# Optimization experiments

Measured on AMD Instinct MI355X. Metric: run time of the kernel, lower is better.

The kernel has to match this reference:

```python
import jax, jax.numpy as jnp
import numpy as np

SCALES = (32.0, 64.0, 128.0, 256.0)
RATIOS = (0.5, 1.0, 2.0)
STRIDE = 16
KEEP = 2000          # pre-NMS top-k
TOPK = 300           # post-NMS top-k
MIN_SIZE = 16.0
SCORE_THRESH = 0.05
NMS_THRESH = 0.7


def static_anchors():
    a = []
    for s in SCALES:
        for r in RATIOS:
            w = s * r ** 0.5
            h = s / r ** 0.5
            a.append((-w / 2, -h / 2, w / 2, h / 2))
    return jnp.asarray(a, jnp.float32)  # [12,4]


def generate_anchors(h, w):
    base = static_anchors()
    sx = jnp.arange(w, dtype=jnp.float32) * STRIDE + STRIDE / 2
    sy = jnp.arange(h, dtype=jnp.float32) * STRIDE + STRIDE / 2
    yy, xx = jnp.meshgrid(sy, sx, indexing='ij')
    xs, ys = xx.reshape(-1), yy.reshape(-1)
    shifts = jnp.stack((xs, ys, xs, ys), axis=1)            # [HW,4]
    return (base[None, :, :] + shifts[:, None, :]).reshape(-1, 4)  # [HW*12,4]


def apply_deltas(anchors, d):
    # bbox reg weights are all 1.0
    aw = anchors[..., 2] - anchors[..., 0]
    ah = anchors[..., 3] - anchors[..., 1]
    ax = anchors[..., 0] + aw * 0.5
    ay = anchors[..., 1] + ah * 0.5
    x = ax + d[..., 0] * aw
    y = ay + d[..., 1] * ah
    w = aw * jnp.exp(d[..., 2])
    h = ah * jnp.exp(d[..., 3])
    return jnp.stack((x - w * 0.5, y - h * 0.5, x + w * 0.5, y + h * 0.5), axis=-1)


def conv2d(x, w, b, pad):
    y = jax.lax.conv_general_dilated(x, w, (1, 1), [(pad, pad), (pad, pad)],
                                     dimension_numbers=('NCHW', 'OIHW', 'NCHW'))
    return y + b[None, :, None, None]


def nms_fixed(boxes, scores, valid):
    # boxes already sorted by descending score; greedy NMS with fixed shapes.
    area = (boxes[:, 2] - boxes[:, 0]) * (boxes[:, 3] - boxes[:, 1])
    lt = jnp.maximum(boxes[:, None, :2], boxes[None, :, :2])
    rb = jnp.minimum(boxes[:, None, 2:], boxes[None, :, 2:])
    wh = jnp.clip(rb - lt, 0.0)
    inter = wh[..., 0] * wh[..., 1]
    iou = inter / jnp.maximum(area[:, None] + area[None, :] - inter, 1e-6)
    n = boxes.shape[0]

    def body(i, state):
        keep, supp = state
        k = jnp.logical_and(~supp[i], True)
        keep = keep.at[i].set(k)
        supp = jnp.logical_or(supp, jnp.logical_and(k, iou[i] > NMS_THRESH))
        return keep, supp

    keep, _ = jax.lax.fori_loop(0, n, body, (jnp.zeros(n, bool), ~valid))
    masked = jnp.where(keep, scores, -jnp.inf)
    top_s, top_i = jax.lax.top_k(masked, TOPK)
    ok = top_s > -jnp.inf
    out_boxes = jnp.where(ok[:, None], boxes[top_i], 0.0)
    out_scores = jnp.where(ok, top_s, 0.0)
    return out_boxes, out_scores


def rpn_forward(fx, w1, b1, w2, b2, w3, b3, img_h, img_w):
    _, _, H, W = fx.shape
    x = jax.nn.relu(conv2d(fx, w1, b1, 1))        # [1,512,H,W]
    ox = conv2d(x, w2, b2, 0)                     # [1,12,H,W]
    ax = conv2d(x, w3, b3, 0)                     # [1,48,H,W]
    anchors = generate_anchors(H, W)              # [A,4]
    ox = jnp.transpose(ox, (0, 2, 3, 1)).reshape(-1)                     # [A]
    ax = jnp.transpose(ax.reshape(1, 12, 4, H, W), (0, 3, 4, 1, 2)).reshape(-1, 4)  # [A,4]
    px = apply_deltas(anchors, ax)                # [A,4]
    s = jax.nn.sigmoid(ox)
    top_s, idx = jax.lax.top_k(s, KEEP)           # pre-NMS filter
    b = px[idx]
    x1 = jnp.clip(b[:, 0], 0.0, img_w)
    x2 = jnp.clip(b[:, 2], 0.0, img_w)
    y1 = jnp.clip(b[:, 1], 0.0, img_h)
    y2 = jnp.clip(b[:, 3], 0.0, img_h)
    boxes = jnp.stack((x1, y1, x2, y2), axis=1)
    valid = ((x2 - x1) >= MIN_SIZE) & ((y2 - y1) >= MIN_SIZE) & (top_s >= SCORE_THRESH)
    out_boxes, out_scores = nms_fixed(boxes, top_s, valid)
    return jnp.concatenate((out_boxes, out_scores[:, None]), axis=1)  # [TOPK,5]


def setup_inputs() -> dict:
    key = jax.random.key(0)
    ks = jax.random.split(key, 4)
    fx = jax.random.normal(ks[0], (1, 1024, 64, 64), jnp.float32)
    w1 = jax.random.normal(ks[1], (512, 1024, 3, 3), jnp.float32) * 0.01
    w2 = jax.random.normal(ks[2], (12, 512, 1, 1), jnp.float32) * 0.01
    w3 = jax.random.normal(ks[3], (48, 512, 1, 1), jnp.float32) * 0.01
    return {"fx": fx, "w1": w1, "b1": jnp.zeros((512,), jnp.float32),
            "w2": w2, "b2": jnp.zeros((12,), jnp.float32),
            "w3": w3, "b3": jnp.zeros((48,), jnp.float32),
            "img_h": 1024, "img_w": 1024}


def reference(fx, w1, b1, w2, b2, w3, b3, img_h, img_w):
    return rpn_forward(fx, w1, b1, w2, b2, w3, b3, float(img_h), float(img_w))
```

## Files before the change

### kernel.cpp

```cpp
#include <hip/hip_runtime.h>
#include <math.h>

typedef unsigned int u32;
typedef unsigned long long u64;
typedef unsigned short u16;

typedef float f32x16 __attribute__((ext_vector_type(16)));
typedef short bf16x8 __attribute__((ext_vector_type(8)));

#define A_TOTAL 49152
#define NKEEP 2000
#define NTOPK 300
#define SORTN 4096

#define OFF_PACC   0u
#define OFF_POX    8388608u
#define OFF_BOXES  16777216u
#define OFF_SCORES 17563648u
#define OFF_HIST   17760256u
#define OFF_KEYS   18022400u
#define OFF_CAND5  18055168u
#define OFF_MASK   18096128u
#define OFF_MISC   18620416u

__global__ __launch_bounds__(256) void k_init(u32* __restrict__ hist, u64* __restrict__ keys,
                                              u32* __restrict__ misc, float* __restrict__ out) {
    int t = blockIdx.x * 256 + threadIdx.x;
    if (t < 65536) hist[t] = 0u;
    if (t < SORTN) keys[t] = 0ull;
    if (t < NTOPK * 5) out[t] = 0.f;
    if (t == 0) misc[0] = 0u;
}

__device__ __forceinline__ u16 f2bf(float v) {
    u32 u = __float_as_uint(v);
    return (u16)((u + 0x7FFFu + ((u >> 16) & 1u)) >> 16);
}
__device__ __forceinline__ float bf2f(u16 h) { return __uint_as_float(((u32)h) << 16); }
__device__ __forceinline__ void split3(float v, u16& h, u16& m, u16& l) {
    h = f2bf(v);
    float r1 = v - bf2f(h);
    m = f2bf(r1);
    float r2 = r1 - bf2f(m);
    l = f2bf(r2);
}
__device__ __forceinline__ bf16x8 ldsfrag(const u16* p) {
    const u64* q = (const u64*)p;
    union { u64 w[2]; bf16x8 v; } x;
    x.w[0] = q[0];
    x.w[1] = q[1];
    return x.v;
}

__global__ __launch_bounds__(512) void k_conv1m(const float* __restrict__ fx, const float* __restrict__ w1,
                                                float* __restrict__ pacc) {
    __shared__ u16 sA[3 * 9472];
    __shared__ u16 sB[3 * 3600];
    u32* const sA32 = (u32*)sA;
    const int tid = threadIdx.x;
    const int lane = tid & 63;
    const int wid = tid >> 6;
    const int cgw = wid >> 2;
    const int pgw = wid & 3;
    const int n = lane & 31;
    const int g = lane >> 5;
    const int bid = blockIdx.x;
    const int yb = bid & 7;
    const int rest = bid >> 3;
    const int bpx = rest & 31;
    const int kh = rest >> 5;
    const int y0 = (bpx >> 2) * 8, x0 = (bpx & 3) * 16;
    const int co0 = yb * 64;
    const int ci_base = kh * 512;

    int wgp[9], wlp[9];
#pragma unroll
    for (int j = 0; j < 9; j++) {
        int p = tid + j * 512;
        int co = p / 72, q = p - co * 72;
        int a = q & 7, b = q >> 3;
        wgp[j] = co * 9216 + (2 * a) * 9 + b;
        wlp[j] = co * 74 + b * 8 + a;
    }
    int fg0[6], fl[6];
#pragma unroll
    for (int j = 0; j < 6; j++) {
        int idx = tid + j * 512;
        bool wr = idx < 2880;
        int ci = idx / 180, rem = idx - ci * 180;
        int hy = rem / 18, hx = rem - hy * 18;
        int gy = y0 + hy - 1, gx = x0 + hx - 1;
        bool ok = wr && gy >= 0 && gy < 64 && gx >= 0 && gx < 64;
        fg0[j] = ok ? (ci * 4096 + gy * 64 + gx) : -1;
        fl[j] = wr ? (rem * 20 + ci) : -1;
    }

    f32x16 acc;
    double accD[16];
#pragma unroll
    for (int i = 0; i < 16; i++) { acc[i] = 0.f; accD[i] = 0.0; }

    float pw[18], pfA[6], pfB[6];
    {
        const float* wp = w1 + (size_t)co0 * 9216 + (size_t)ci_base * 9;
#pragma unroll
        for (int j = 0; j < 9; j++) { pw[2 * j] = wp[wgp[j]]; pw[2 * j + 1] = wp[wgp[j] + 9]; }
        const float* f0 = fx + (size_t)ci_base * 4096;
        const float* f1 = fx + (size_t)(ci_base + 16) * 4096;
#pragma unroll
        for (int j = 0; j < 6; j++) {
            pfA[j] = (fg0[j] >= 0) ? f0[fg0[j]] : 0.f;
            pfB[j] = (fg0[j] >= 0) ? f1[fg0[j]] : 0.f;
        }
    }

#pragma unroll 1
    for (int c = 0; c < 32; c++) {
        __syncthreads();
#pragma unroll
        for (int j = 0; j < 9; j++) {
            u16 h0, m0, l0, h1, m1, l1;
            split3(pw[2 * j], h0, m0, l0);
            split3(pw[2 * j + 1], h1, m1, l1);
            sA32[wlp[j]] = (u32)h0 | ((u32)h1 << 16);
            sA32[4736 + wlp[j]] = (u32)m0 | ((u32)m1 << 16);
            sA32[9472 + wlp[j]] = (u32)l0 | ((u32)l1 << 16);
        }
#pragma unroll
        for (int j = 0; j < 6; j++) {
            if (fl[j] >= 0) {
                u16 h, m, l;
                split3(pfA[j], h, m, l);
                sB[fl[j]] = h; sB[3600 + fl[j]] = m; sB[7200 + fl[j]] = l;
            }
        }
        __syncthreads();
        if (c < 31) {
            const float* wp = w1 + (size_t)co0 * 9216 + (size_t)(ci_base + (c + 1) * 16) * 9;
#pragma unroll
            for (int j = 0; j < 9; j++) { pw[2 * j] = wp[wgp[j]]; pw[2 * j + 1] = wp[wgp[j] + 9]; }
        }
#pragma unroll
        for (int j = 0; j < 6; j++) pfA[j] = pfB[j];
        if (c < 30) {
            const float* fp = fx + (size_t)(ci_base + (c + 2) * 16) * 4096;
#pragma unroll
            for (int j = 0; j < 6; j++) pfB[j] = (fg0[j] >= 0) ? fp[fg0[j]] : 0.f;
        }

#pragma unroll 1
        for (int dy = 0; dy < 3; dy++) {
#pragma unroll
            for (int dx = 0; dx < 3; dx++) {
                const int tap = dy * 3 + dx;
                const int aoff = (cgw * 32 + n) * 148 + tap * 16 + g * 8;
                bf16x8 ah = ldsfrag(&sA[aoff]);
                bf16x8 am = ldsfrag(&sA[9472 + aoff]);
                bf16x8 al = ldsfrag(&sA[18944 + aoff]);
                const int loc = (pgw * 2 + (n >> 4) + dy) * 18 + (n & 15) + dx;
                const int boff = loc * 20 + g * 8;
                bf16x8 bh = ldsfrag(&sB[boff]);
                bf16x8 bm = ldsfrag(&sB[3600 + boff]);
                bf16x8 bl = ldsfrag(&sB[7200 + boff]);
                acc = __builtin_amdgcn_mfma_f32_32x32x16_bf16(ah, bh, acc, 0, 0, 0);
                acc = __builtin_amdgcn_mfma_f32_32x32x16_bf16(ah, bm, acc, 0, 0, 0);
                acc = __builtin_amdgcn_mfma_f32_32x32x16_bf16(am, bh, acc, 0, 0, 0);
                acc = __builtin_amdgcn_mfma_f32_32x32x16_bf16(ah, bl, acc, 0, 0, 0);
                acc = __builtin_amdgcn_mfma_f32_32x32x16_bf16(am, bm, acc, 0, 0, 0);
                acc = __builtin_amdgcn_mfma_f32_32x32x16_bf16(al, bh, acc, 0, 0, 0);
            }
#pragma unroll
            for (int i = 0; i < 16; i++) { accD[i] += (double)acc[i]; acc[i] = 0.f; }
        }
    }

    {
        int p = pgw * 32 + n;
        int py = p >> 4, pxx = p & 15;
        int gp = (y0 + py) * 64 + x0 + pxx;
        const int row_hi = 4 * g;
#pragma unroll
        for (int rg = 0; rg < 16; rg++) {
            int co = co0 + cgw * 32 + (rg & 3) + 8 * (rg >> 2) + row_hi;
            pacc[(size_t)kh * 2097152 + (size_t)co * 4096 + gp] = (float)accD[rg];
        }
    }
}

__global__ __launch_bounds__(256) void k_comb(float* __restrict__ x, const float* __restrict__ p1,
                                              const float* __restrict__ b1) {
    int i = blockIdx.x * 256 + threadIdx.x;
    double v = (double)x[i] + (double)p1[i] + (double)b1[i >> 12];
    x[i] = fmaxf((float)v, 0.f);
}

__global__ __launch_bounds__(256) void k_conv23(const float* __restrict__ x,
                                                const float* __restrict__ w2, const float* __restrict__ w3,
                                                double* __restrict__ pox) {
    __shared__ float xs[32 * 64];
    __shared__ float wsh[60 * 128];
    const int tid = threadIdx.x;
    const int px0 = blockIdx.x * 64;
    const int cib = blockIdx.y * 128;
    const int px = tid & 63;
    const int og = tid >> 6;

#pragma unroll
    for (int k = 0; k < 30; k++) {
        int e = tid + k * 256;
        int o = e >> 7, ci = e & 127;
        float wv = (o < 12) ? w2[o * 512 + cib + ci] : w3[(size_t)(o - 12) * 512 + cib + ci];
        wsh[o * 128 + ci] = wv;
    }

    double acc[15];
#pragma unroll
    for (int j = 0; j < 15; j++) acc[j] = 0.0;

#pragma unroll 1
    for (int ch = 0; ch < 4; ch++) {
        __syncthreads();
#pragma unroll
        for (int k = 0; k < 8; k++) {
            int e = tid + k * 256;
            int ci = e >> 6, p = e & 63;
            xs[ci * 64 + p] = x[(size_t)(cib + ch * 32 + ci) * 4096 + px0 + p];
        }
        __syncthreads();
#pragma unroll 1
        for (int ci = 0; ci < 32; ci++) {
            double xd = (double)xs[ci * 64 + px];
            const float* wrow = &wsh[ch * 32 + ci];
#pragma unroll
            for (int j = 0; j < 15; j++)
                acc[j] = fma(xd, (double)wrow[(og * 15 + j) * 128], acc[j]);
        }
    }
#pragma unroll
    for (int j = 0; j < 15; j++) {
        int o = og * 15 + j;
        pox[((size_t)o * 4 + blockIdx.y) * 4096 + px0 + px] = acc[j];
    }
}

__global__ __launch_bounds__(256) void k_boxes(const double* __restrict__ pox,
                                               const float* __restrict__ b2, const float* __restrict__ b3,
                                               const int* __restrict__ imh, const int* __restrict__ imw,
                                               float* __restrict__ boxes, float* __restrict__ scores,
                                               u32* __restrict__ hist) {
    int idx = blockIdx.x * 256 + threadIdx.x;
    if (idx >= A_TOTAL) return;
    int px = idx / 12, a = idx - px * 12;

    double t = 0.0;
#pragma unroll
    for (int q = 0; q < 4; q++) t += pox[((size_t)a * 4 + q) * 4096 + px];
    float o = (float)(t + (double)b2[a]);
    float s = (float)(1.0 / (1.0 + exp(-(double)o)));
    scores[idx] = s;
    atomicAdd(&hist[__float_as_uint(s) >> 16], 1u);

    float d[4];
#pragma unroll
    for (int c = 0; c < 4; c++) {
        int oo = 12 + a * 4 + c;
        double u = 0.0;
#pragma unroll
        for (int q = 0; q < 4; q++) u += pox[((size_t)oo * 4 + q) * 4096 + px];
        d[c] = (float)(u + (double)b3[a * 4 + c]);
    }

    int py = px >> 6, pxx = px & 63;
    double cx = pxx * 16.0 + 8.0, cy = py * 16.0 + 8.0;
    int si = a / 3, ri = a - si * 3;
    double scale = (double)(32 << si);
    double ratio = 0.5 * (double)(1 << ri);
    double sq = sqrt(ratio);
    double aw = scale * sq, ah = scale / sq;
    double xc = cx + (double)d[0] * aw;
    double yc = cy + (double)d[1] * ah;
    double wv = aw * exp((double)d[2]);
    double hv = ah * exp((double)d[3]);
    float W = (float)imw[0], H = (float)imh[0];
    float x1 = fminf(fmaxf((float)(xc - wv * 0.5), 0.f), W);
    float x2 = fminf(fmaxf((float)(xc + wv * 0.5), 0.f), W);
    float y1 = fminf(fmaxf((float)(yc - hv * 0.5), 0.f), H);
    float y2 = fminf(fmaxf((float)(yc + hv * 0.5), 0.f), H);
    boxes[(size_t)idx * 4 + 0] = x1;
    boxes[(size_t)idx * 4 + 1] = y1;
    boxes[(size_t)idx * 4 + 2] = x2;
    boxes[(size_t)idx * 4 + 3] = y2;
}

__global__ __launch_bounds__(256) void k_scanhist(const u32* __restrict__ hist, u32* __restrict__ misc) {
    __shared__ u32 csum[256];
    __shared__ u32 cb[256];
    __shared__ int s_cidx;
    __shared__ u32 s_cacc;
    int t = threadIdx.x;
    u32 sum = 0;
    const uint4* h4 = (const uint4*)(hist + t * 256);
    for (int j = 0; j < 64; j++) { uint4 v = h4[j]; sum += v.x + v.y + v.z + v.w; }
    csum[t] = sum;
    __syncthreads();
    if (t == 0) {
        u32 acc = 0;
        int c = 255;
        for (; c > 0; c--) {
            if (acc + csum[c] >= NKEEP) break;
            acc += csum[c];
        }
        s_cidx = c;
        s_cacc = acc;
    }
    __syncthreads();
    cb[t] = hist[s_cidx * 256 + t];
    __syncthreads();
    if (t == 0) {
        u32 acc = s_cacc;
        int b = 255;
        for (; b > 0; b--) {
            acc += cb[b];
            if (acc >= NKEEP) break;
        }
        misc[1] = (u32)(s_cidx * 256 + b);
    }
}

__global__ __launch_bounds__(256) void k_compact(const float* __restrict__ scores, u32* __restrict__ misc,
                                                 u64* __restrict__ keys) {
    int idx = blockIdx.x * 256 + threadIdx.x;
    if (idx >= A_TOTAL) return;
    u32 bits = __float_as_uint(scores[idx]);
    if ((bits >> 16) >= misc[1]) {
        u32 slot = atomicAdd(&misc[0], 1u);
        if (slot < SORTN) keys[slot] = ((u64)bits << 32) | (u64)(~(u32)idx);
    }
}

__global__ __launch_bounds__(1024) void k_sort(const u64* __restrict__ keys, const float* __restrict__ boxes,
                                               float* __restrict__ cand5, u64* __restrict__ suppws) {
    __shared__ u64 lk[SORTN];
    int t = threadIdx.x;
#pragma unroll
    for (int r = 0; r < 4; r++) lk[r * 1024 + t] = keys[r * 1024 + t];
    for (int kk = 2; kk <= SORTN; kk <<= 1) {
        for (int jj = kk >> 1; jj > 0; jj >>= 1) {
            __syncthreads();
#pragma unroll
            for (int rep = 0; rep < 4; rep++) {
                int i = rep * 1024 + t;
                int ixj = i ^ jj;
                if (ixj > i) {
                    u64 a = lk[i], b = lk[ixj];
                    bool sw = ((i & kk) == 0) ? (a < b) : (a > b);
                    if (sw) { lk[i] = b; lk[ixj] = a; }
                }
            }
        }
    }
    __syncthreads();
#pragma unroll
    for (int rep = 0; rep < 2; rep++) {
        int i = rep * 1024 + t;
        bool suppb = true;
        float c0 = 0.f, c1 = 0.f, c2 = 0.f, c3 = 0.f, cs = 0.f;
        if (i < NKEEP) {
            u64 key = lk[i];
            u32 idx = ~(u32)(key & 0xFFFFFFFFull);
            cs = __uint_as_float((u32)(key >> 32));
            c0 = boxes[(size_t)idx * 4 + 0];
            c1 = boxes[(size_t)idx * 4 + 1];
            c2 = boxes[(size_t)idx * 4 + 2];
            c3 = boxes[(size_t)idx * 4 + 3];
            bool valid = ((c2 - c0) >= 16.f) && ((c3 - c1) >= 16.f) && (cs >= 0.05f);
            suppb = !valid;
        }
        cand5[i * 5 + 0] = c0;
        cand5[i * 5 + 1] = c1;
        cand5[i * 5 + 2] = c2;
        cand5[i * 5 + 3] = c3;
        cand5[i * 5 + 4] = cs;
        u64 bal = __ballot(suppb ? 1 : 0);
        if ((t & 63) == 0) suppws[i >> 6] = bal;
    }
}

__global__ __launch_bounds__(64) void k_mask(const float* __restrict__ cand5, u64* __restrict__ mask) {
    __shared__ float cb[64][5];
    int t = threadIdx.x;
    int bi = blockIdx.y, bj = blockIdx.x;
    int j = bj * 64 + t;
    {
        float b0 = cand5[j * 5 + 0], b1v = cand5[j * 5 + 1], b2v = cand5[j * 5 + 2], b3v = cand5[j * 5 + 3];
        cb[t][0] = b0; cb[t][1] = b1v; cb[t][2] = b2v; cb[t][3] = b3v;
        cb[t][4] = (b2v - b0) * (b3v - b1v);
    }
    __syncthreads();
    int i = bi * 64 + t;
    float r0 = cand5[i * 5 + 0], r1 = cand5[i * 5 + 1], r2 = cand5[i * 5 + 2], r3 = cand5[i * 5 + 3];
    float ra = (r2 - r0) * (r3 - r1);
    u64 bits = 0ull;
#pragma unroll 4
    for (int c = 0; c < 64; c++) {
        float lx = fmaxf(r0, cb[c][0]);
        float ly = fmaxf(r1, cb[c][1]);
        float rx = fminf(r2, cb[c][2]);
        float ry = fminf(r3, cb[c][3]);
        float w = fmaxf(rx - lx, 0.f);
        float h = fmaxf(ry - ly, 0.f);
        float inter = w * h;
        float iou = inter / fmaxf(ra + cb[c][4] - inter, 1e-6f);
        if (iou > 0.7f) bits |= (1ull << c);
    }
    mask[(size_t)i * 32 + bj] = bits;
}

__global__ __launch_bounds__(64) void k_scan(const u64* __restrict__ mask, const float* __restrict__ cand5,
                                             const u64* __restrict__ suppws, float* __restrict__ out) {
    int lane = threadIdx.x;
    u64 supp = (lane < 32) ? suppws[lane] : 0ull;
    u64 bufA[8], bufB[8];
    float dA[8], dB[8];
#pragma unroll
    for (int k = 0; k < 8; k++) {
        bufA[k] = (lane < 32) ? mask[(size_t)k * 32 + lane] : 0ull;
        dA[k] = (lane < 5) ? cand5[k * 5 + lane] : 0.f;
    }
    int kcount = 0;
    for (int gq = 0; gq < 256; gq++) {
        int base = gq * 8;
        if (gq < 255) {
            int nb = base + 8;
#pragma unroll
            for (int k = 0; k < 8; k++) {
                bufB[k] = (lane < 32) ? mask[(size_t)(nb + k) * 32 + lane] : 0ull;
                dB[k] = (lane < 5) ? cand5[(nb + k) * 5 + lane] : 0.f;
            }
        }
        int w = gq >> 3;
        u64 cur = __shfl(supp, w);
#pragma unroll
        for (int k = 0; k < 8; k++) {
            int i = base + k;
            if (i < NKEEP && !((cur >> (i & 63)) & 1ull)) {
                if (kcount < NTOPK) {
                    if (lane < 5) out[kcount * 5 + lane] = dA[k];
                    kcount++;
                }
                supp |= bufA[k];
                cur |= __shfl(bufA[k], w);
            }
        }
        if (kcount >= NTOPK) return;
#pragma unroll
        for (int k = 0; k < 8; k++) { bufA[k] = bufB[k]; dA[k] = dB[k]; }
    }
}

extern "C" void kernel_launch(void* const* d_in, const int* in_sizes, int n_in,
                              void* d_out, int out_size, void* d_ws, size_t ws_size,
                              hipStream_t stream) {
    (void)in_sizes; (void)n_in; (void)out_size; (void)ws_size;
    const float* fx = (const float*)d_in[0];
    const float* w1 = (const float*)d_in[1];
    const float* b1 = (const float*)d_in[2];
    const float* w2 = (const float*)d_in[3];
    const float* b2 = (const float*)d_in[4];
    const float* w3 = (const float*)d_in[5];
    const float* b3 = (const float*)d_in[6];
    const int* imh = (const int*)d_in[7];
    const int* imw = (const int*)d_in[8];

    char* ws = (char*)d_ws;
    float*  pacc   = (float*)(ws + OFF_PACC);
    double* pox    = (double*)(ws + OFF_POX);
    float*  boxes  = (float*)(ws + OFF_BOXES);
    float*  scores = (float*)(ws + OFF_SCORES);
    u32*    hist   = (u32*)(ws + OFF_HIST);
    u64*    keys   = (u64*)(ws + OFF_KEYS);
    float*  cand5  = (float*)(ws + OFF_CAND5);
    u64*    mask   = (u64*)(ws + OFF_MASK);
    u32*    misc   = (u32*)(ws + OFF_MISC);
    u64*    suppws = (u64*)(ws + OFF_MISC + 64);
    float*  out    = (float*)d_out;

    k_init<<<256, 256, 0, stream>>>(hist, keys, misc, out);
    k_conv1m<<<512, 512, 0, stream>>>(fx, w1, pacc);
    k_comb<<<8192, 256, 0, stream>>>(pacc, pacc + 2097152, b1);
    k_conv23<<<dim3(64, 4), 256, 0, stream>>>(pacc, w2, w3, pox);
    k_boxes<<<192, 256, 0, stream>>>(pox, b2, b3, imh, imw, boxes, scores, hist);
    k_scanhist<<<1, 256, 0, stream>>>(hist, misc);
    k_compact<<<192, 256, 0, stream>>>(scores, misc, keys);
    k_sort<<<1, 1024, 0, stream>>>(keys, boxes, cand5, suppws);
    k_mask<<<dim3(32, 32), 64, 0, stream>>>(cand5, mask);
    k_scan<<<1, 64, 0, stream>>>(mask, cand5, suppws, out);
}
```

Before: 554.8 us.

## Pre-split conv weights into bf16 triples and stream them to LDS directly

Adds a pre-pass kernel that splits the 3x3 conv weights into hi/mid/lo bf16 parts once per call, laid out in the tile order the conv kernel consumes. The main conv kernel then copies these tiles into LDS with global_load_lds instead of loading fp32 weights and splitting them in every block. This removes the repeated splitting and register staging of weights from the conv loop. The cost is an extra kernel launch and about 28 MB of workspace traffic. A fallback to the old kernel runs when the workspace is too small.

```diff
diff --git a/kernel.cpp b/kernel.cpp
--- a/kernel.cpp
+++ b/kernel.cpp
@@ -22,6 +22,8 @@
 #define OFF_CAND5  18055168u
 #define OFF_MASK   18096128u
 #define OFF_MISC   18620416u
+#define OFF_PREW   18624512u
+#define WS_NEED    46936064ull
 
 __global__ __launch_bounds__(256) void k_init(u32* __restrict__ hist, u64* __restrict__ keys,
                                               u32* __restrict__ misc, float* __restrict__ out) {
@@ -51,9 +53,172 @@
     x.w[1] = q[1];
     return x.v;
 }
-
-__global__ __launch_bounds__(512) void k_conv1m(const float* __restrict__ fx, const float* __restrict__ w1,
+__device__ __forceinline__ void gll16(const void* g, void* l) {
+    __builtin_amdgcn_global_load_lds((const __attribute__((address_space(1))) void*)g,
+                                     (__attribute__((address_space(3))) void*)l, 16, 0, 0);
+}
+__device__ __forceinline__ void gll4(const void* g, void* l) {
+    __builtin_amdgcn_global_load_lds((const __attribute__((address_space(1))) void*)g,
+                                     (__attribute__((address_space(3))) void*)l, 4, 0, 0);
+}
+
+__global__ __launch_bounds__(256) void k_splitw(const float* __restrict__ w1, uint4* __restrict__ preW) {
+    int u = blockIdx.x * 256 + threadIdx.x;
+    int co = u & 63;
+    int r1 = u >> 6;
+    int g = r1 & 1;
+    int r2 = r1 >> 1;
+    int tap = r2 % 9;
+    int r3 = r2 / 9;
+    int c = r3 & 31;
+    int r4 = r3 >> 5;
+    int yb = r4 & 7;
+    int kh = r4 >> 3;
+    int ci0 = kh * 512 + c * 16 + g * 8;
+    const float* wp = w1 + (size_t)(yb * 64 + co) * 9216 + (size_t)ci0 * 9 + tap;
+    union { u16 q[8]; uint4 v; } H, M, L;
+#pragma unroll
+    for (int i = 0; i < 8; i++) {
+        u16 h, m, l;
+        split3(wp[i * 9], h, m, l);
+        H.q[i] = h; M.q[i] = m; L.q[i] = l;
+    }
+    size_t base = (size_t)(((kh * 8 + yb) * 32 + c) * 3) * 1152 + (size_t)((tap * 2 + g) * 64 + co);
+    preW[base] = H.v;
+    preW[base + 1152] = M.v;
+    preW[base + 2304] = L.v;
+}
+
+__global__ __launch_bounds__(512) void k_conv1m(const float* __restrict__ fx, const uint4* __restrict__ preW,
                                                 float* __restrict__ pacc) {
+    __shared__ __align__(16) u16 sA[3 * 9216];
+    __shared__ __align__(16) u16 sB[3 * 3600];
+    u32* const sB32 = (u32*)sB;
+    const int tid = threadIdx.x;
+    const int lane = tid & 63;
+    const int wid = tid >> 6;
+    const int cgw = wid >> 2;
+    const int pgw = wid & 3;
+    const int n = lane & 31;
+    const int g = lane >> 5;
+    const int bid = blockIdx.x;
+    const int yb = bid & 7;
+    const int rest = bid >> 3;
+    const int bpx = rest & 31;
+    const int kh = rest >> 5;
+    const int y0 = (bpx >> 2) * 8, x0 = (bpx & 3) * 16;
+    const int ci_base = kh * 512;
+
+    int fgp[3], flp[3];
+    bool wrp[3], ldp[3];
+#pragma unroll
+    for (int j = 0; j < 3; j++) {
+        int p = tid + j * 512;
+        bool wr = p < 1440;
+        int a = p / 180, rem = p - a * 180;
+        int hy = rem / 18, hx = rem - hy * 18;
+        int gy = y0 + hy - 1, gx = x0 + hx - 1;
+        bool ok = wr && gy >= 0 && gy < 64 && gx >= 0 && gx < 64;
+        wrp[j] = wr;
+        ldp[j] = ok;
+        fgp[j] = ok ? ((2 * a) * 4096 + gy * 64 + gx) : 0;
+        flp[j] = wr ? (rem * 10 + a) : 0;
+    }
+
+    f32x16 acc;
+    double accD[16];
+#pragma unroll
+    for (int i = 0; i < 16; i++) { acc[i] = 0.f; accD[i] = 0.0; }
+
+    float pA0[3], pA1[3], pB0[3], pB1[3];
+    {
+        const float* f0 = fx + (size_t)ci_base * 4096;
+        const float* f1 = fx + (size_t)(ci_base + 16) * 4096;
+#pragma unroll
+        for (int j = 0; j < 3; j++) {
+            pA0[j] = ldp[j] ? f0[fgp[j]] : 0.f;
+            pA1[j] = ldp[j] ? f0[fgp[j] + 4096] : 0.f;
+            pB0[j] = ldp[j] ? f1[fgp[j]] : 0.f;
+            pB1[j] = ldp[j] ? f1[fgp[j] + 4096] : 0.f;
+        }
+    }
+    const char* wbase = (const char*)preW + (size_t)((kh * 8 + yb) * 32) * 3 * 18432;
+    char* const sAc = (char*)sA;
+
+#pragma unroll 1
+    for (int c = 0; c < 32; c++) {
+        __syncthreads();
+        const char* wsrc = wbase + (size_t)c * 3 * 18432;
+#pragma unroll
+        for (int s = 0; s < 3; s++) {
+            gll16(wsrc + s * 18432 + tid * 16,         sAc + s * 18432 + wid * 1024);
+            gll16(wsrc + s * 18432 + 8192 + tid * 16,  sAc + s * 18432 + 8192 + wid * 1024);
+            gll4 (wsrc + s * 18432 + 16384 + tid * 4,  sAc + s * 18432 + 16384 + wid * 256);
+        }
+#pragma unroll
+        for (int j = 0; j < 3; j++) {
+            if (wrp[j]) {
+                u16 h0, m0, l0, h1, m1, l1;
+                split3(pA0[j], h0, m0, l0);
+                split3(pA1[j], h1, m1, l1);
+                sB32[flp[j]] = (u32)h0 | ((u32)h1 << 16);
+                sB32[1800 + flp[j]] = (u32)m0 | ((u32)m1 << 16);
+                sB32[3600 + flp[j]] = (u32)l0 | ((u32)l1 << 16);
+            }
+        }
+        __syncthreads();
+#pragma unroll
+        for (int j = 0; j < 3; j++) { pA0[j] = pB0[j]; pA1[j] = pB1[j]; }
+        if (c < 30) {
+            const float* fp = fx + (size_t)(ci_base + (c + 2) * 16) * 4096;
+#pragma unroll
+            for (int j = 0; j < 3; j++) {
+                pB0[j] = ldp[j] ? fp[fgp[j]] : 0.f;
+                pB1[j] = ldp[j] ? fp[fgp[j] + 4096] : 0.f;
+            }
+        }
+
+#pragma unroll 1
+        for (int dy = 0; dy < 3; dy++) {
+#pragma unroll
+            for (int dx = 0; dx < 3; dx++) {
+                const int tap = dy * 3 + dx;
+                const int aoff = ((tap * 2 + g) * 64 + cgw * 32 + n) * 8;
+                bf16x8 ah = ldsfrag(&sA[aoff]);
+                bf16x8 am = ldsfrag(&sA[9216 + aoff]);
+                bf16x8 al = ldsfrag(&sA[18432 + aoff]);
+                const int loc = (pgw * 2 + (n >> 4) + dy) * 18 + (n & 15) + dx;
+                const int boff = loc * 20 + g * 8;
+                bf16x8 bh = ldsfrag(&sB[boff]);
+                bf16x8 bm = ldsfrag(&sB[3600 + boff]);
+                bf16x8 bl = ldsfrag(&sB[7200 + boff]);
+                acc = __builtin_amdgcn_mfma_f32_32x32x16_bf16(ah, bh, acc, 0, 0, 0);
+                acc = __builtin_amdgcn_mfma_f32_32x32x16_bf16(ah, bm, acc, 0, 0, 0);
+                acc = __builtin_amdgcn_mfma_f32_32x32x16_bf16(am, bh, acc, 0, 0, 0);
+                acc = __builtin_amdgcn_mfma_f32_32x32x16_bf16(ah, bl, acc, 0, 0, 0);
+                acc = __builtin_amdgcn_mfma_f32_32x32x16_bf16(am, bm, acc, 0, 0, 0);
+                acc = __builtin_amdgcn_mfma_f32_32x32x16_bf16(al, bh, acc, 0, 0, 0);
+            }
+#pragma unroll
+            for (int i = 0; i < 16; i++) { accD[i] += (double)acc[i]; acc[i] = 0.f; }
+        }
+    }
+
+    {
+        int p = pgw * 32 + n;
+        int py = p >> 4, pxx = p & 15;
+        int gp = (y0 + py) * 64 + x0 + pxx;
+        const int row_hi = 4 * g;
+#pragma unroll
+        for (int rg = 0; rg < 16; rg++) {
+            int co = yb * 64 + cgw * 32 + (rg & 3) + 8 * (rg >> 2) + row_hi;
+            pacc[(size_t)kh * 2097152 + (size_t)co * 4096 + gp] = (float)accD[rg];
+        }
+    }
+}
+
+__global__ __launch_bounds__(512) void k_conv1m_fb(const float* __restrict__ fx, const float* __restrict__ w1,
+                                                   float* __restrict__ pacc) {
     __shared__ u16 sA[3 * 9472];
     __shared__ u16 sB[3 * 3600];
     u32* const sA32 = (u32*)sA;
@@ -461,7 +626,7 @@
 extern "C" void kernel_launch(void* const* d_in, const int* in_sizes, int n_in,
                               void* d_out, int out_size, void* d_ws, size_t ws_size,
                               hipStream_t stream) {
-    (void)in_sizes; (void)n_in; (void)out_size; (void)ws_size;
+    (void)in_sizes; (void)n_in; (void)out_size;
     const float* fx = (const float*)d_in[0];
     const float* w1 = (const float*)d_in[1];
     const float* b1 = (const float*)d_in[2];
@@ -483,10 +648,16 @@
     u64*    mask   = (u64*)(ws + OFF_MASK);
     u32*    misc   = (u32*)(ws + OFF_MISC);
     u64*    suppws = (u64*)(ws + OFF_MISC + 64);
+    uint4*  preW   = (uint4*)(ws + OFF_PREW);
     float*  out    = (float*)d_out;
 
     k_init<<<256, 256, 0, stream>>>(hist, keys, misc, out);
-    k_conv1m<<<512, 512, 0, stream>>>(fx, w1, pacc);
+    if (ws_size >= WS_NEED) {
+        k_splitw<<<2304, 256, 0, stream>>>(w1, preW);
+        k_conv1m<<<512, 512, 0, stream>>>(fx, preW, pacc);
+    } else {
+        k_conv1m_fb<<<512, 512, 0, stream>>>(fx, w1, pacc);
+    }
     k_comb<<<8192, 256, 0, stream>>>(pacc, pacc + 2097152, b1);
     k_conv23<<<dim3(64, 4), 256, 0, stream>>>(pacc, w2, w3, pox);
     k_boxes<<<192, 256, 0, stream>>>(pox, b2, b3, imh, imw, boxes, scores, hist);
```

New measurement: 481.4 us. -13.2%, faster.
